# Kernel optimization log

Hardware: AMD Instinct MI355X
Metric: run time of the kernel (lower is better)

Reference implementation:

```python
import jax, jax.numpy as jnp
import numpy as np

B, S, D_IN, UNITS = 4, 4096, 256, 64


def setup_inputs() -> dict:
    key = jax.random.key(0)
    ks = jax.random.split(key, 4)
    scale = 1.0 / np.sqrt(D_IN)
    return {
        "x": jax.random.normal(ks[0], (B, S, D_IN), dtype=jnp.float32),
        "Wq": jax.random.normal(ks[1], (D_IN, UNITS), dtype=jnp.float32) * scale,
        "bq": jnp.zeros((UNITS,), dtype=jnp.float32),
        "Wk": jax.random.normal(ks[2], (D_IN, UNITS), dtype=jnp.float32) * scale,
        "bk": jnp.zeros((UNITS,), dtype=jnp.float32),
        "Wv": jax.random.normal(ks[3], (D_IN, UNITS), dtype=jnp.float32) * scale,
        "bv": jnp.zeros((UNITS,), dtype=jnp.float32),
    }


def reference(x, Wq, bq, Wk, bk, Wv, bv):
    # Q/K/V projections: [B, S, D_IN] @ [D_IN, UNITS] -> [B, S, UNITS]
    q = jnp.einsum("bsd,du->bsu", x, Wq) + bq
    k = jnp.einsum("bsd,du->bsu", x, Wk) + bk
    v = jnp.einsum("bsd,du->bsu", x, Wv) + bv
    # Full [B, S, S] scores (the module materializes these - headroom target)
    sims = jnp.einsum("bsu,btu->bst", q, k) / np.sqrt(UNITS).astype(np.float32)
    attn = jax.nn.softmax(sims, axis=-1)
    out = jnp.einsum("bst,btu->bsu", attn, v)
    return out  # activation is None (linear)
```

## Files before the change

kernel.cpp:

```cpp
#include <hip/hip_runtime.h>
#include <hip/hip_bf16.h>

#define B_ 4
#define S_ 4096
#define D_ 256
#define U_ 64
#define NROWS (B_ * S_)
#define QSCALE 0.1803368801111244f

typedef __attribute__((ext_vector_type(8))) short short8;
typedef __attribute__((ext_vector_type(8))) float float8;
typedef __attribute__((ext_vector_type(4))) float floatx4;

__device__ inline short f2bf(float f) {
    union { __hip_bfloat16 h; short s; } u;
    u.h = __float2bfloat16(f);
    return u.s;
}
__device__ inline unsigned pk2bf(float a, float b) {
    unsigned ua = __float_as_uint(a) + 0x8000u;
    unsigned ub = __float_as_uint(b) + 0x8000u;
    return (ub & 0xFFFF0000u) | (ua >> 16);
}

__global__ void pack_w_kernel(const float* __restrict__ Wq,
                              const float* __restrict__ Wk,
                              const float* __restrict__ Wv,
                              short* __restrict__ wpack) {
    int tid = blockIdx.x * 256 + threadIdx.x;
    if (tid >= 3 * 16384) return;
    int p = tid >> 14, e = tid & 16383;
    const float* W = (p == 0) ? Wq : (p == 1) ? Wk : Wv;
    float w = W[e];
    int k = e >> 6, n = e & 63;
    int ks = k >> 5, hi = (k >> 3) & 3, j = k & 7;
    int l = hi * 16 + (n & 15), nc = n >> 4;
    wpack[p * 16384 + ((ks * 4 + nc) * 64 + l) * 8 + j] = f2bf(w);
}

__global__ __launch_bounds__(256) void qkv_proj_kernel(
    const float* __restrict__ x, const short* __restrict__ wpack,
    const float* __restrict__ bq, const float* __restrict__ bk,
    const float* __restrict__ bv,
    short* __restrict__ Q, short* __restrict__ Kpack, short* __restrict__ Vpack) {
    __shared__ __align__(16) short k_sh[64][72];
    __shared__ __align__(16) short vT_sh[64][72];
    const int wl    = threadIdx.x >> 6;
    const int lane  = threadIdx.x & 63;
    const int col16 = lane & 15, quad = lane >> 4;
    const int m0b = blockIdx.x * 64, m0 = m0b + wl * 16;

    floatx4 acc[3][4];
#pragma unroll
    for (int p = 0; p < 3; ++p)
#pragma unroll
        for (int nc = 0; nc < 4; ++nc) acc[p][nc] = (floatx4){0.f, 0.f, 0.f, 0.f};

    const float* xrow = x + (size_t)(m0 + col16) * D_ + quad * 8;
#pragma unroll
    for (int ks = 0; ks < 8; ++ks) {
        float8 af = *(const float8*)(xrow + ks * 32);
        short8 a;
#pragma unroll
        for (int j = 0; j < 8; ++j) a[j] = f2bf(af[j]);
#pragma unroll
        for (int p = 0; p < 3; ++p) {
#pragma unroll
            for (int nc = 0; nc < 4; ++nc) {
                short8 bfr = *(const short8*)(wpack +
                    ((size_t)((p * 8 + ks) * 4 + nc) * 64 + lane) * 8);
                acc[p][nc] = __builtin_amdgcn_mfma_f32_16x16x32_bf16(a, bfr, acc[p][nc], 0, 0, 0);
            }
        }
    }

#pragma unroll
    for (int nc = 0; nc < 4; ++nc) {
        float biasq = bq[nc * 16 + col16];
        float biask = bk[nc * 16 + col16];
        float biasv = bv[nc * 16 + col16];
#pragma unroll
        for (int r = 0; r < 4; ++r) {
            int row = m0 + quad * 4 + r;
            Q[(size_t)row * U_ + nc * 16 + col16] = f2bf((acc[0][nc][r] + biasq) * QSCALE);
            k_sh[wl * 16 + quad * 4 + r][nc * 16 + col16] = f2bf(acc[1][nc][r] + biask);
        }
        union { short s[4]; unsigned long long u; } pv;
#pragma unroll
        for (int r = 0; r < 4; ++r) pv.s[r] = f2bf(acc[2][nc][r] + biasv);
        *(unsigned long long*)&vT_sh[nc * 16 + col16][wl * 16 + quad * 4] = pv.u;
    }
    __syncthreads();

#pragma unroll
    for (int c2 = 0; c2 < 2; ++c2) {
        int combo = wl + c2 * 4;
        int ww = combo >> 2, t = (combo >> 1) & 1, h = combo & 1;
        int srow = ww * 32 + (col16 >> 2) * 8 + (col16 & 3) + 4 * t;
        short8 v = *(const short8*)&k_sh[srow][h * 32 + quad * 8];
        size_t gt = (size_t)blockIdx.x * 2 + ww;
        *(short8*)(Kpack + (gt * 4 + t * 2 + h) * 512 + lane * 8) = v;
    }
#pragma unroll
    for (int c2 = 0; c2 < 2; ++c2) {
        int combo = wl + c2 * 4;
        int ww = combo >> 2, nc = combo & 3;
        short8 v = *(const short8*)&vT_sh[nc * 16 + col16][ww * 32 + quad * 8];
        size_t gt = (size_t)blockIdx.x * 2 + ww;
        *(short8*)(Vpack + (gt * 4 + nc) * 512 + lane * 8) = v;
    }
}

__global__ __launch_bounds__(512) void attn_kernel(
    const short* __restrict__ Q, const short* __restrict__ Kpack,
    const short* __restrict__ Vpack, float* __restrict__ out) {
    __shared__ float o_sh[4][32][65];
    __shared__ float l_sh[8][2][16];

    const int b  = blockIdx.y;
    const int q0 = blockIdx.x * 32;
    const int kw = threadIdx.x >> 6;
    const int lane  = threadIdx.x & 63;
    const int col16 = lane & 15, quad = lane >> 4;

    const short* Qb = Q + (size_t)b * S_ * U_;

    short8 bQ[2][2];
#pragma unroll
    for (int qs = 0; qs < 2; ++qs) {
        const short* qrow = Qb + (size_t)(q0 + qs * 16 + col16) * U_ + quad * 8;
        bQ[qs][0] = *(const short8*)(qrow);
        bQ[qs][1] = *(const short8*)(qrow + 32);
    }

    floatx4 o[2][4];
#pragma unroll
    for (int qs = 0; qs < 2; ++qs)
#pragma unroll
        for (int nc = 0; nc < 4; ++nc) o[qs][nc] = (floatx4){0.f, 0.f, 0.f, 0.f};
    float l_i[2] = {0.f, 0.f};

    const short* kbase = Kpack + ((size_t)(b * 128 + kw * 16)) * 2048 + lane * 8;
    const short* vbase = Vpack + ((size_t)(b * 128 + kw * 16)) * 2048 + lane * 8;

    for (int it = 0; it < 16; ++it) {
        const short* kp = kbase + it * 2048;
        const short* vp = vbase + it * 2048;
        short8 ak[2][2];
#pragma unroll
        for (int t = 0; t < 2; ++t)
#pragma unroll
            for (int h = 0; h < 2; ++h)
                ak[t][h] = *(const short8*)(kp + (t * 2 + h) * 512);
        short8 av[4];
#pragma unroll
        for (int nc = 0; nc < 4; ++nc)
            av[nc] = *(const short8*)(vp + nc * 512);

        floatx4 c[2][2];
#pragma unroll
        for (int t = 0; t < 2; ++t)
#pragma unroll
            for (int qs = 0; qs < 2; ++qs) {
                c[t][qs] = __builtin_amdgcn_mfma_f32_16x16x32_bf16(ak[t][0], bQ[qs][0],
                              (floatx4){0.f, 0.f, 0.f, 0.f}, 0, 0, 0);
                c[t][qs] = __builtin_amdgcn_mfma_f32_16x16x32_bf16(ak[t][1], bQ[qs][1], c[t][qs], 0, 0, 0);
            }

#pragma unroll
        for (int qs = 0; qs < 2; ++qs) {
            float p[8];
            float rs = 0.f;
#pragma unroll
            for (int t = 0; t < 2; ++t)
#pragma unroll
                for (int r = 0; r < 4; ++r) {
                    float e = exp2f(c[t][qs][r]);
                    p[t * 4 + r] = e;
                    rs += e;
                }
            l_i[qs] += rs;
            union { short8 s; unsigned u[4]; } pb;
            pb.u[0] = pk2bf(p[0], p[1]);
            pb.u[1] = pk2bf(p[2], p[3]);
            pb.u[2] = pk2bf(p[4], p[5]);
            pb.u[3] = pk2bf(p[6], p[7]);
#pragma unroll
            for (int nc = 0; nc < 4; ++nc)
                o[qs][nc] = __builtin_amdgcn_mfma_f32_16x16x32_bf16(av[nc], pb.s, o[qs][nc], 0, 0, 0);
        }
    }

#pragma unroll
    for (int qs = 0; qs < 2; ++qs) {
        l_i[qs] += __shfl_xor(l_i[qs], 16, 64);
        l_i[qs] += __shfl_xor(l_i[qs], 32, 64);
    }
    if (quad == 0) {
#pragma unroll
        for (int qs = 0; qs < 2; ++qs) l_sh[kw][qs][col16] = l_i[qs];
    }

    if (kw < 4) {
#pragma unroll
        for (int qs = 0; qs < 2; ++qs)
#pragma unroll
            for (int nc = 0; nc < 4; ++nc)
#pragma unroll
                for (int r = 0; r < 4; ++r)
                    o_sh[kw][qs * 16 + col16][nc * 16 + quad * 4 + r] = o[qs][nc][r];
    }
    __syncthreads();
    if (kw >= 4) {
#pragma unroll
        for (int qs = 0; qs < 2; ++qs)
#pragma unroll
            for (int nc = 0; nc < 4; ++nc)
#pragma unroll
                for (int r = 0; r < 4; ++r)
                    o_sh[kw - 4][qs * 16 + col16][nc * 16 + quad * 4 + r] += o[qs][nc][r];
    }
    __syncthreads();
    for (int i = threadIdx.x; i < 32 * 64; i += 512) {
        int row = i >> 6, col = i & 63;
        int qs2 = row >> 4, c = row & 15;
        float lt = 0.f;
#pragma unroll
        for (int ww = 0; ww < 8; ++ww) lt += l_sh[ww][qs2][c];
        float s = o_sh[0][row][col] + o_sh[1][row][col]
                + o_sh[2][row][col] + o_sh[3][row][col];
        out[((size_t)b * S_ + q0 + row) * U_ + col] = s / lt;
    }
}

extern "C" void kernel_launch(void* const* d_in, const int* in_sizes, int n_in,
                              void* d_out, int out_size, void* d_ws, size_t ws_size,
                              hipStream_t stream) {
    const float* x  = (const float*)d_in[0];
    const float* Wq = (const float*)d_in[1];
    const float* bq = (const float*)d_in[2];
    const float* Wk = (const float*)d_in[3];
    const float* bk = (const float*)d_in[4];
    const float* Wv = (const float*)d_in[5];
    const float* bv = (const float*)d_in[6];
    float* out = (float*)d_out;

    short* Q     = (short*)d_ws;
    short* Kpack = Q + (size_t)NROWS * U_;
    short* Vpack = Kpack + (size_t)NROWS * U_;
    short* wpack = Vpack + (size_t)NROWS * U_;

    pack_w_kernel<<<192, 256, 0, stream>>>(Wq, Wk, Wv, wpack);
    qkv_proj_kernel<<<NROWS / 64, 256, 0, stream>>>(
        x, wpack, bq, bk, bv, Q, Kpack, Vpack);
    attn_kernel<<<dim3(S_ / 32, B_), 512, 0, stream>>>(Q, Kpack, Vpack, out);
}
```

Before: 114.1 us.

## Process 64 query rows per attention block to reuse K/V loads

Each attention workgroup now handles 64 query rows instead of 32, so every K/V fragment loaded from global memory feeds four query sub-tiles rather than two. This halves total K/V traffic and the grid size, now 256 blocks. The cross-wave output reduction is restructured into a four-stage shared-memory accumulation with extra barriers. In exchange, register pressure per thread rises from the doubled accumulators, and fewer blocks may leave compute units underused.

```diff
diff --git a/kernel.cpp b/kernel.cpp
--- a/kernel.cpp
+++ b/kernel.cpp
@@ -114,31 +114,31 @@
 __global__ __launch_bounds__(512) void attn_kernel(
     const short* __restrict__ Q, const short* __restrict__ Kpack,
     const short* __restrict__ Vpack, float* __restrict__ out) {
-    __shared__ float o_sh[4][32][65];
-    __shared__ float l_sh[8][2][16];
+    __shared__ float o_sh[2][64][65];
+    __shared__ float l_sh[8][4][16];
 
     const int b  = blockIdx.y;
-    const int q0 = blockIdx.x * 32;
+    const int q0 = blockIdx.x * 64;
     const int kw = threadIdx.x >> 6;
     const int lane  = threadIdx.x & 63;
     const int col16 = lane & 15, quad = lane >> 4;
 
     const short* Qb = Q + (size_t)b * S_ * U_;
 
-    short8 bQ[2][2];
-#pragma unroll
-    for (int qs = 0; qs < 2; ++qs) {
+    short8 bQ[4][2];
+#pragma unroll
+    for (int qs = 0; qs < 4; ++qs) {
         const short* qrow = Qb + (size_t)(q0 + qs * 16 + col16) * U_ + quad * 8;
         bQ[qs][0] = *(const short8*)(qrow);
         bQ[qs][1] = *(const short8*)(qrow + 32);
     }
 
-    floatx4 o[2][4];
-#pragma unroll
-    for (int qs = 0; qs < 2; ++qs)
+    floatx4 o[4][4];
+#pragma unroll
+    for (int qs = 0; qs < 4; ++qs)
 #pragma unroll
         for (int nc = 0; nc < 4; ++nc) o[qs][nc] = (floatx4){0.f, 0.f, 0.f, 0.f};
-    float l_i[2] = {0.f, 0.f};
+    float l_i[4] = {0.f, 0.f, 0.f, 0.f};
 
     const short* kbase = Kpack + ((size_t)(b * 128 + kw * 16)) * 2048 + lane * 8;
     const short* vbase = Vpack + ((size_t)(b * 128 + kw * 16)) * 2048 + lane * 8;
@@ -157,25 +157,22 @@
         for (int nc = 0; nc < 4; ++nc)
             av[nc] = *(const short8*)(vp + nc * 512);
 
-        floatx4 c[2][2];
-#pragma unroll
-        for (int t = 0; t < 2; ++t)
-#pragma unroll
-            for (int qs = 0; qs < 2; ++qs) {
-                c[t][qs] = __builtin_amdgcn_mfma_f32_16x16x32_bf16(ak[t][0], bQ[qs][0],
-                              (floatx4){0.f, 0.f, 0.f, 0.f}, 0, 0, 0);
-                c[t][qs] = __builtin_amdgcn_mfma_f32_16x16x32_bf16(ak[t][1], bQ[qs][1], c[t][qs], 0, 0, 0);
+#pragma unroll
+        for (int qs = 0; qs < 4; ++qs) {
+            floatx4 c[2];
+#pragma unroll
+            for (int t = 0; t < 2; ++t) {
+                c[t] = __builtin_amdgcn_mfma_f32_16x16x32_bf16(ak[t][0], bQ[qs][0],
+                          (floatx4){0.f, 0.f, 0.f, 0.f}, 0, 0, 0);
+                c[t] = __builtin_amdgcn_mfma_f32_16x16x32_bf16(ak[t][1], bQ[qs][1], c[t], 0, 0, 0);
             }
-
-#pragma unroll
-        for (int qs = 0; qs < 2; ++qs) {
             float p[8];
             float rs = 0.f;
 #pragma unroll
             for (int t = 0; t < 2; ++t)
 #pragma unroll
                 for (int r = 0; r < 4; ++r) {
-                    float e = exp2f(c[t][qs][r]);
+                    float e = exp2f(c[t][r]);
                     p[t * 4 + r] = e;
                     rs += e;
                 }
@@ -192,18 +189,18 @@
     }
 
 #pragma unroll
-    for (int qs = 0; qs < 2; ++qs) {
+    for (int qs = 0; qs < 4; ++qs) {
         l_i[qs] += __shfl_xor(l_i[qs], 16, 64);
         l_i[qs] += __shfl_xor(l_i[qs], 32, 64);
     }
     if (quad == 0) {
 #pragma unroll
-        for (int qs = 0; qs < 2; ++qs) l_sh[kw][qs][col16] = l_i[qs];
-    }
-
-    if (kw < 4) {
-#pragma unroll
-        for (int qs = 0; qs < 2; ++qs)
+        for (int qs = 0; qs < 4; ++qs) l_sh[kw][qs][col16] = l_i[qs];
+    }
+
+    if (kw < 2) {
+#pragma unroll
+        for (int qs = 0; qs < 4; ++qs)
 #pragma unroll
             for (int nc = 0; nc < 4; ++nc)
 #pragma unroll
@@ -211,9 +208,19 @@
                     o_sh[kw][qs * 16 + col16][nc * 16 + quad * 4 + r] = o[qs][nc][r];
     }
     __syncthreads();
-    if (kw >= 4) {
-#pragma unroll
-        for (int qs = 0; qs < 2; ++qs)
+    if (kw == 2 || kw == 3) {
+#pragma unroll
+        for (int qs = 0; qs < 4; ++qs)
+#pragma unroll
+            for (int nc = 0; nc < 4; ++nc)
+#pragma unroll
+                for (int r = 0; r < 4; ++r)
+                    o_sh[kw - 2][qs * 16 + col16][nc * 16 + quad * 4 + r] += o[qs][nc][r];
+    }
+    __syncthreads();
+    if (kw == 4 || kw == 5) {
+#pragma unroll
+        for (int qs = 0; qs < 4; ++qs)
 #pragma unroll
             for (int nc = 0; nc < 4; ++nc)
 #pragma unroll
@@ -221,14 +228,23 @@
                     o_sh[kw - 4][qs * 16 + col16][nc * 16 + quad * 4 + r] += o[qs][nc][r];
     }
     __syncthreads();
-    for (int i = threadIdx.x; i < 32 * 64; i += 512) {
+    if (kw >= 6) {
+#pragma unroll
+        for (int qs = 0; qs < 4; ++qs)
+#pragma unroll
+            for (int nc = 0; nc < 4; ++nc)
+#pragma unroll
+                for (int r = 0; r < 4; ++r)
+                    o_sh[kw - 6][qs * 16 + col16][nc * 16 + quad * 4 + r] += o[qs][nc][r];
+    }
+    __syncthreads();
+    for (int i = threadIdx.x; i < 64 * 64; i += 512) {
         int row = i >> 6, col = i & 63;
         int qs2 = row >> 4, c = row & 15;
         float lt = 0.f;
 #pragma unroll
         for (int ww = 0; ww < 8; ++ww) lt += l_sh[ww][qs2][c];
-        float s = o_sh[0][row][col] + o_sh[1][row][col]
-                + o_sh[2][row][col] + o_sh[3][row][col];
+        float s = o_sh[0][row][col] + o_sh[1][row][col];
         out[((size_t)b * S_ + q0 + row) * U_ + col] = s / lt;
     }
 }
@@ -253,5 +269,5 @@
     pack_w_kernel<<<192, 256, 0, stream>>>(Wq, Wk, Wv, wpack);
     qkv_proj_kernel<<<NROWS / 64, 256, 0, stream>>>(
         x, wpack, bq, bk, bv, Q, Kpack, Vpack);
-    attn_kernel<<<dim3(S_ / 32, B_), 512, 0, stream>>>(Q, Kpack, Vpack, out);
-}
+    attn_kernel<<<dim3(S_ / 64, B_), 512, 0, stream>>>(Q, Kpack, Vpack, out);
+}
```

Result: slower. 120.7 us (+5.8%).
